# Kernel tuning notes

Measured on AMD Instinct MI355X. Metric: run time of the kernel, lower is better.

The kernel has to match this reference:

```python
import jax, jax.numpy as jnp
import numpy as np

N = 100000   # nodes
E = 1280000  # edges (avg degree ~12.8)
D = 64       # feature / hidden channels


def _init_linear(key, fan_in, fan_out):
    # Kaiming-uniform-ish init like torch Linear
    bound = 1.0 / np.sqrt(fan_in)
    return jax.random.uniform(key, (fan_in, fan_out), minval=-bound, maxval=bound)


def setup_inputs() -> dict:
    key = jax.random.key(0)
    ks = jax.random.split(key, 16)
    inp = {
        "x": jax.random.normal(ks[0], (N, D), dtype=jnp.float32),
        "edge_index": jax.random.randint(ks[1], (2, E), 0, N, dtype=jnp.int32),
        "edge_weight": jax.random.uniform(ks[2], (E,), dtype=jnp.float32),
        "batch": jnp.zeros((N,), dtype=jnp.int32),
    }
    # GraphConv params per layer: lin_rel (weight+bias) applied to aggregated
    # neighbor sum, lin_root (weight, no bias) applied to the node itself.
    for i, k in zip((1, 2, 3), range(3, 12, 3)):
        inp[f"W_rel{i}"] = _init_linear(ks[k], D, D)
        inp[f"b_rel{i}"] = jnp.zeros((D,), dtype=jnp.float32)
        inp[f"W_root{i}"] = _init_linear(ks[k + 1], D, D)
    return inp


def _graph_conv(x, src, dst, w, W_rel, b_rel, W_root):
    # message: w_ij * x_j, aggregated (sum) at target nodes
    msg = w[:, None] * x[src]                                  # [E, D]
    agg = jax.ops.segment_sum(msg, dst, num_segments=N)       # [N, D]
    return agg @ W_rel + b_rel + x @ W_root                   # [N, D]


def reference(x, edge_index, edge_weight, batch,
              W_rel1, b_rel1, W_root1,
              W_rel2, b_rel2, W_root2,
              W_rel3, b_rel3, W_root3):
    src, dst = edge_index[0], edge_index[1]
    h = jax.nn.relu(_graph_conv(x, src, dst, edge_weight, W_rel1, b_rel1, W_root1))
    h = jax.nn.relu(_graph_conv(h, src, dst, edge_weight, W_rel2, b_rel2, W_root2))
    h = _graph_conv(h, src, dst, edge_weight, W_rel3, b_rel3, W_root3)
    return h
```

## Files before the change

kernel.cpp:

```cpp
#include <hip/hip_runtime.h>
#include <hip/hip_bf16.h>

#define NN 100000
#define NE 1280000
#define DD 64
#define RSHIFT 9
#define NRANGE 196

typedef __attribute__((ext_vector_type(8))) short bf16x8;
typedef __attribute__((ext_vector_type(4))) float f32x4;

static __device__ __forceinline__ unsigned short f2bf(float f) {
    __hip_bfloat16 h = __float2bfloat16(f);
    return *reinterpret_cast<unsigned short*>(&h);
}

__global__ __launch_bounds__(256) void f32_to_bf16_kernel(
    const float* __restrict__ in, unsigned short* __restrict__ out)
{
    int i = (blockIdx.x * 256 + threadIdx.x) * 4;
    float4 v = *(const float4*)(in + i);
    ushort4 o;
    o.x = f2bf(v.x); o.y = f2bf(v.y); o.z = f2bf(v.z); o.w = f2bf(v.w);
    *(ushort4*)(out + i) = o;
}

__global__ __launch_bounds__(256) void bpack_kernel(
    const float* __restrict__ Wrel1, const float* __restrict__ Wroot1,
    const float* __restrict__ Wrel2, const float* __restrict__ Wroot2,
    const float* __restrict__ Wrel3, const float* __restrict__ Wroot3,
    unsigned short* __restrict__ Bp)
{
    int L = blockIdx.x;
    const float* Wrel  = (L == 0) ? Wrel1  : (L == 1) ? Wrel2  : Wrel3;
    const float* Wroot = (L == 0) ? Wroot1 : (L == 1) ? Wroot2 : Wroot3;
    int tid = threadIdx.x;
    int wv = tid >> 6, lane = tid & 63, quad = lane >> 4, m16 = lane & 15;
    int n = wv * 16 + m16;
    unsigned short* o = Bp + (size_t)L * 4 * 256 * 8;
#pragma unroll
    for (int t = 0; t < 4; ++t)
#pragma unroll
        for (int j = 0; j < 8; ++j) {
            int k = t * 32 + quad * 8 + j;
            float wval = (k < 64) ? Wrel[k * 64 + n] : Wroot[(k - 64) * 64 + n];
            o[((size_t)t * 256 + tid) * 8 + j] = f2bf(wval);
        }
}

__global__ __launch_bounds__(256) void hist2_kernel(
    const int* __restrict__ dst, int* __restrict__ rangeCnt)
{
    __shared__ int h[256];
    int tid = threadIdx.x;
    h[tid] = 0;
    __syncthreads();
    int e0 = blockIdx.x * 1024 + tid * 4;
    int4 d4 = *(const int4*)(dst + e0);
    atomicAdd(&h[d4.x >> RSHIFT], 1);
    atomicAdd(&h[d4.y >> RSHIFT], 1);
    atomicAdd(&h[d4.z >> RSHIFT], 1);
    atomicAdd(&h[d4.w >> RSHIFT], 1);
    __syncthreads();
    if (tid < NRANGE && h[tid]) atomicAdd(&rangeCnt[tid], h[tid]);
}

__global__ __launch_bounds__(256) void scan196_kernel(
    const int* __restrict__ rangeCnt, int* __restrict__ rangeBase,
    int* __restrict__ gcur, int* __restrict__ rowptr)
{
    __shared__ int sd[256];
    int tid = threadIdx.x;
    int v = (tid < NRANGE) ? rangeCnt[tid] : 0;
    sd[tid] = v;
    __syncthreads();
    for (int o = 1; o < 256; o <<= 1) {
        int t = (tid >= o) ? sd[tid - o] : 0;
        __syncthreads();
        sd[tid] += t;
        __syncthreads();
    }
    if (tid < NRANGE) { int ex = sd[tid] - v; rangeBase[tid] = ex; gcur[tid] = ex; }
    if (tid == 0) { rangeBase[NRANGE] = NE; rowptr[NN] = NE; }
}

__global__ __launch_bounds__(256) void p1_bin_kernel(
    const int* __restrict__ src, const int* __restrict__ dst,
    const float* __restrict__ w, int* __restrict__ gcur,
    int2* __restrict__ ecoarse)
{
    __shared__ int2 stage[1024];
    __shared__ unsigned char sbkt[1024];
    __shared__ int cnt[256], ofs[256], gpos[256], sd[256];

    int tid = threadIdx.x;
    int e0 = blockIdx.x * 1024 + tid * 4;
    int4   s4 = *(const int4*)(src + e0);
    int4   d4 = *(const int4*)(dst + e0);
    float4 w4 = *(const float4*)(w + e0);

    cnt[tid] = 0;
    __syncthreads();

    int ss[4] = {s4.x, s4.y, s4.z, s4.w};
    int dd[4] = {d4.x, d4.y, d4.z, d4.w};
    float ww[4] = {w4.x, w4.y, w4.z, w4.w};
    int b[4], p[4];
#pragma unroll
    for (int i = 0; i < 4; ++i) {
        b[i] = dd[i] >> RSHIFT;
        p[i] = atomicAdd(&cnt[b[i]], 1);
    }
    __syncthreads();

    int cv = cnt[tid];
    sd[tid] = cv;
    __syncthreads();
    for (int o = 1; o < 256; o <<= 1) {
        int t = (tid >= o) ? sd[tid - o] : 0;
        __syncthreads();
        sd[tid] += t;
        __syncthreads();
    }
    ofs[tid] = sd[tid] - cv;
    if (tid < NRANGE && cv > 0) gpos[tid] = atomicAdd(&gcur[tid], cv);
    __syncthreads();

#pragma unroll
    for (int i = 0; i < 4; ++i) {
        int slot = ofs[b[i]] + p[i];
        stage[slot] = make_int2(ss[i] | ((dd[i] & 511) << 17), __float_as_int(ww[i]));
        sbkt[slot] = (unsigned char)b[i];
    }
    __syncthreads();

    for (int j = tid; j < 1024; j += 256) {
        int bb = sbkt[j];
        ecoarse[gpos[bb] + (j - ofs[bb])] = stage[j];
    }
}

__global__ __launch_bounds__(256) void p2_place_kernel(
    const int2* __restrict__ ecoarse, const int* __restrict__ rangeBase,
    int* __restrict__ rowptr, int2* __restrict__ ebuf)
{
    __shared__ int cnt[512];
    __shared__ int ssum[256];
    int r = blockIdx.x, tid = threadIdx.x;
    int beg = rangeBase[r], end = rangeBase[r + 1];

    cnt[tid] = 0; cnt[tid + 256] = 0;
    __syncthreads();

    for (int j = beg + tid; j < end; j += 256) {
        int2 rec = ecoarse[j];
        atomicAdd(&cnt[(rec.x >> 17) & 511], 1);
    }
    __syncthreads();

    int c0 = cnt[2 * tid], c1 = cnt[2 * tid + 1];
    int s = c0 + c1;
    ssum[tid] = s;
    __syncthreads();
    for (int o = 1; o < 256; o <<= 1) {
        int t = (tid >= o) ? ssum[tid - o] : 0;
        __syncthreads();
        ssum[tid] += t;
        __syncthreads();
    }
    int p0 = beg + ssum[tid] - s;
    int p1 = p0 + c0;

    int node0 = (r << RSHIFT) + 2 * tid;
    if (node0 < NN)     rowptr[node0]     = p0;
    if (node0 + 1 < NN) rowptr[node0 + 1] = p1;
    cnt[2 * tid] = p0; cnt[2 * tid + 1] = p1;
    __syncthreads();

    for (int j = beg + tid; j < end; j += 256) {
        int2 rec = ecoarse[j];
        int dl = (rec.x >> 17) & 511;
        int p = atomicAdd(&cnt[dl], 1);
        ebuf[p] = make_int2(rec.x & 0x1FFFF, rec.y);
    }
}

template <bool RELU, bool OUT32>
__global__ __launch_bounds__(512) void fused_layer_kernel(
    const unsigned short* __restrict__ hb,
    const int* __restrict__ rowptr,
    const int2* __restrict__ ebuf,
    const unsigned short* __restrict__ Bp,
    const float* __restrict__ brel,
    void* __restrict__ outp)
{
    __shared__ __align__(16) unsigned int AstW[4 * 256];

    int tid = threadIdx.x;
    int lane = tid & 63;
    int wv = tid >> 6;
    int half = lane >> 5;
    int ch = lane & 31;
    int base = blockIdx.x * 16;
    int node = base + wv * 2 + half;

    const unsigned int* __restrict__ hw = (const unsigned int*)hb;

    bf16x8 bfrag[4];
    float bias = 0.f;
    if (wv < 4) {
#pragma unroll
        for (int t2 = 0; t2 < 4; ++t2)
            bfrag[t2] = *(const bf16x8*)(Bp + ((size_t)t2 * 256 + tid) * 8);
        bias = brel[(wv << 4) | (lane & 15)];
    }

    unsigned rootp = hw[(size_t)node * 32 + ch];

    int beg = rowptr[node];
    int end = rowptr[node + 1];
    int deg = end - beg;

    float aL0 = 0.f, aH0 = 0.f, aL1 = 0.f, aH1 = 0.f;
    for (int c = 0; c < deg; c += 32) {
        int rem = deg - c;
        int nsl = rem < 32 ? rem : 32;
        int idx = (ch < nsl) ? (c + ch) : c;
        int2 e = ebuf[beg + idx];
        float wt = (ch < nsl) ? __int_as_float(e.y) : 0.f;

        for (int s0 = 0; s0 < nsl; s0 += 8) {
#pragma unroll
            for (int i = 0; i < 8; ++i) {
                int slot = s0 + i;
                bool ok = slot < nsl;
                int sl = (half << 5) | (ok ? slot : 0);
                int sr = __shfl(e.x, sl);
                float w = __shfl(wt, sl);
                w = ok ? w : 0.f;
                unsigned v = hw[(size_t)sr * 32 + ch];
                if (i & 1) {
                    aL1 = fmaf(w, __uint_as_float(v << 16), aL1);
                    aH1 = fmaf(w, __uint_as_float(v & 0xFFFF0000u), aH1);
                } else {
                    aL0 = fmaf(w, __uint_as_float(v << 16), aL0);
                    aH0 = fmaf(w, __uint_as_float(v & 0xFFFF0000u), aH0);
                }
            }
        }
    }
    float accL = aL0 + aL1, accH = aH0 + aH1;

    int m = wv * 2 + half;
    int t = ch >> 4, q = (ch >> 2) & 3, jj = ch & 3;
    unsigned pack = ((unsigned)f2bf(accH) << 16) | (unsigned)f2bf(accL);
    AstW[t * 256 + (q * 16 + m) * 4 + jj] = pack;
    AstW[(2 + t) * 256 + (q * 16 + m) * 4 + jj] = rootp;
    __syncthreads();

    if (wv < 4) {
        int quad = lane >> 4, m16 = lane & 15;
        int n = wv * 16 + m16;
        f32x4 cacc = {0.f, 0.f, 0.f, 0.f};
#pragma unroll
        for (int t2 = 0; t2 < 4; ++t2) {
            bf16x8 a = *(const bf16x8*)&AstW[t2 * 256 + lane * 4];
            cacc = __builtin_amdgcn_mfma_f32_16x16x32_bf16(a, bfrag[t2], cacc, 0, 0, 0);
        }
#pragma unroll
        for (int reg = 0; reg < 4; ++reg) {
            int row = quad * 4 + reg;
            size_t onode = (size_t)base + row;
            float v2 = cacc[reg] + bias;
            if (RELU) v2 = fmaxf(v2, 0.f);
            if (OUT32) ((float*)outp)[onode * DD + n] = v2;
            else       ((unsigned short*)outp)[onode * DD + n] = f2bf(v2);
        }
    }
}

extern "C" void kernel_launch(void* const* d_in, const int* in_sizes, int n_in,
                              void* d_out, int out_size, void* d_ws, size_t ws_size,
                              hipStream_t stream)
{
    const float* x     = (const float*)d_in[0];
    const int*   ei    = (const int*)d_in[1];
    const float* w     = (const float*)d_in[2];
    const float* Wrel1 = (const float*)d_in[4];
    const float* brel1 = (const float*)d_in[5];
    const float* Wroot1= (const float*)d_in[6];
    const float* Wrel2 = (const float*)d_in[7];
    const float* brel2 = (const float*)d_in[8];
    const float* Wroot2= (const float*)d_in[9];
    const float* Wrel3 = (const float*)d_in[10];
    const float* brel3 = (const float*)d_in[11];
    const float* Wroot3= (const float*)d_in[12];

    float* out = (float*)d_out;

    char* ws = (char*)d_ws;
    int2*  ebuf    = (int2*)ws;                       ws += (size_t)NE * 8;
    int2*  ecoarse = (int2*)ws;
    unsigned short* xb = (unsigned short*)ws;         ws += (size_t)NN * DD * 2;
    unsigned short* hb1 = (unsigned short*)ws;        ws += (size_t)NN * DD * 2;
    unsigned short* hb2 = (unsigned short*)ws;        ws += (size_t)NN * DD * 2;
    int*   rowptr  = (int*)ws;                        ws += (size_t)(NN + 1) * 4;
    int*   rangeCnt = (int*)ws;                       ws += (size_t)256 * 4;
    int*   rangeBase = (int*)ws;                      ws += (size_t)256 * 4;
    int*   gcur    = (int*)ws;                        ws += (size_t)256 * 4;
    unsigned short* Bp = (unsigned short*)ws;

    const int* src = ei;
    const int* dst = ei + NE;

    hipMemsetAsync(rangeCnt, 0, NRANGE * 4, stream);
    bpack_kernel<<<3, 256, 0, stream>>>(Wrel1, Wroot1, Wrel2, Wroot2, Wrel3, Wroot3, Bp);
    hist2_kernel<<<1250, 256, 0, stream>>>(dst, rangeCnt);
    scan196_kernel<<<1, 256, 0, stream>>>(rangeCnt, rangeBase, gcur, rowptr);
    p1_bin_kernel<<<1250, 256, 0, stream>>>(src, dst, w, gcur, ecoarse);
    p2_place_kernel<<<NRANGE, 256, 0, stream>>>(ecoarse, rangeBase, rowptr, ebuf);

    f32_to_bf16_kernel<<<6250, 256, 0, stream>>>(x, xb);

    fused_layer_kernel<true, false><<<NN / 16, 512, 0, stream>>>(
        xb, rowptr, ebuf, Bp, brel1, hb1);
    fused_layer_kernel<true, false><<<NN / 16, 512, 0, stream>>>(
        hb1, rowptr, ebuf, Bp + (size_t)4 * 256 * 8, brel2, hb2);
    fused_layer_kernel<false, true><<<NN / 16, 512, 0, stream>>>(
        hb2, rowptr, ebuf, Bp + (size_t)8 * 256 * 8, brel3, out);
}
```

Measured before the change: 308.4 us.

## Build CSR via global degree atomics, block scan and atomic scatter

Replaces the two-pass coarse-bucket sort with a plain CSR build. The old sort staged edges in LDS and wrote them to an intermediate buffer. The new path counts per-node in-degree with global atomics, then computes row pointers with a two-level block scan. Edges are then scattered straight into their CSR slots using atomic cursors. This removes the intermediate ecoarse pass and its LDS staging, but relies on many contended global atomics and uncoalesced random writes. It also makes edge order within a row nondeterministic.

New measurement: 359.5 us. 16.5% more time.

```diff
diff --git a/kernel.cpp b/kernel.cpp
--- a/kernel.cpp
+++ b/kernel.cpp
@@ -4,8 +4,8 @@
 #define NN 100000
 #define NE 1280000
 #define DD 64
-#define RSHIFT 9
-#define NRANGE 196
+#define NBLK 98
+#define NPAD (NBLK * 1024)
 
 typedef __attribute__((ext_vector_type(8))) short bf16x8;
 typedef __attribute__((ext_vector_type(4))) float f32x4;
@@ -48,141 +48,89 @@
         }
 }
 
-__global__ __launch_bounds__(256) void hist2_kernel(
-    const int* __restrict__ dst, int* __restrict__ rangeCnt)
-{
-    __shared__ int h[256];
-    int tid = threadIdx.x;
-    h[tid] = 0;
-    __syncthreads();
-    int e0 = blockIdx.x * 1024 + tid * 4;
+__global__ __launch_bounds__(256) void degcnt_kernel(
+    const int* __restrict__ dst, int* __restrict__ deg)
+{
+    int e0 = (blockIdx.x * 256 + threadIdx.x) * 4;
     int4 d4 = *(const int4*)(dst + e0);
-    atomicAdd(&h[d4.x >> RSHIFT], 1);
-    atomicAdd(&h[d4.y >> RSHIFT], 1);
-    atomicAdd(&h[d4.z >> RSHIFT], 1);
-    atomicAdd(&h[d4.w >> RSHIFT], 1);
-    __syncthreads();
-    if (tid < NRANGE && h[tid]) atomicAdd(&rangeCnt[tid], h[tid]);
-}
-
-__global__ __launch_bounds__(256) void scan196_kernel(
-    const int* __restrict__ rangeCnt, int* __restrict__ rangeBase,
-    int* __restrict__ gcur, int* __restrict__ rowptr)
+    atomicAdd(&deg[d4.x], 1);
+    atomicAdd(&deg[d4.y], 1);
+    atomicAdd(&deg[d4.z], 1);
+    atomicAdd(&deg[d4.w], 1);
+}
+
+__global__ __launch_bounds__(256) void bsum_kernel(
+    const int* __restrict__ deg, int* __restrict__ bsum)
 {
     __shared__ int sd[256];
     int tid = threadIdx.x;
-    int v = (tid < NRANGE) ? rangeCnt[tid] : 0;
+    int4 c = *(const int4*)(deg + blockIdx.x * 1024 + tid * 4);
+    sd[tid] = c.x + c.y + c.z + c.w;
+    __syncthreads();
+    for (int o = 128; o > 0; o >>= 1) {
+        if (tid < o) sd[tid] += sd[tid + o];
+        __syncthreads();
+    }
+    if (tid == 0) bsum[blockIdx.x] = sd[0];
+}
+
+__global__ __launch_bounds__(128) void scan98_kernel(
+    const int* __restrict__ bsum, int* __restrict__ bbase,
+    int* __restrict__ rowptr)
+{
+    __shared__ int sd[128];
+    int tid = threadIdx.x;
+    int v = (tid < NBLK) ? bsum[tid] : 0;
     sd[tid] = v;
     __syncthreads();
+    for (int o = 1; o < 128; o <<= 1) {
+        int t = (tid >= o) ? sd[tid - o] : 0;
+        __syncthreads();
+        sd[tid] += t;
+        __syncthreads();
+    }
+    if (tid < NBLK) bbase[tid] = sd[tid] - v;
+    if (tid == 0) rowptr[NN] = NE;
+}
+
+__global__ __launch_bounds__(256) void bscan_kernel(
+    const int* __restrict__ deg, const int* __restrict__ bbase,
+    int* __restrict__ rowptr, int* __restrict__ cur)
+{
+    __shared__ int ssum[256];
+    int tid = threadIdx.x;
+    int n0 = blockIdx.x * 1024 + tid * 4;
+    int4 c = *(const int4*)(deg + n0);
+    int s = c.x + c.y + c.z + c.w;
+    ssum[tid] = s;
+    __syncthreads();
     for (int o = 1; o < 256; o <<= 1) {
-        int t = (tid >= o) ? sd[tid - o] : 0;
-        __syncthreads();
-        sd[tid] += t;
-        __syncthreads();
-    }
-    if (tid < NRANGE) { int ex = sd[tid] - v; rangeBase[tid] = ex; gcur[tid] = ex; }
-    if (tid == 0) { rangeBase[NRANGE] = NE; rowptr[NN] = NE; }
-}
-
-__global__ __launch_bounds__(256) void p1_bin_kernel(
+        int t = (tid >= o) ? ssum[tid - o] : 0;
+        __syncthreads();
+        ssum[tid] += t;
+        __syncthreads();
+    }
+    int base = bbase[blockIdx.x] + ssum[tid] - s;
+    int4 r;
+    r.x = base; r.y = base + c.x; r.z = r.y + c.y; r.w = r.z + c.z;
+    *(int4*)(rowptr + n0) = r;
+    *(int4*)(cur + n0) = r;
+}
+
+__global__ __launch_bounds__(256) void scatter_kernel(
     const int* __restrict__ src, const int* __restrict__ dst,
-    const float* __restrict__ w, int* __restrict__ gcur,
-    int2* __restrict__ ecoarse)
-{
-    __shared__ int2 stage[1024];
-    __shared__ unsigned char sbkt[1024];
-    __shared__ int cnt[256], ofs[256], gpos[256], sd[256];
-
-    int tid = threadIdx.x;
-    int e0 = blockIdx.x * 1024 + tid * 4;
+    const float* __restrict__ w, int* __restrict__ cur,
+    int2* __restrict__ ebuf)
+{
+    int e0 = (blockIdx.x * 256 + threadIdx.x) * 4;
     int4   s4 = *(const int4*)(src + e0);
     int4   d4 = *(const int4*)(dst + e0);
     float4 w4 = *(const float4*)(w + e0);
-
-    cnt[tid] = 0;
-    __syncthreads();
-
-    int ss[4] = {s4.x, s4.y, s4.z, s4.w};
-    int dd[4] = {d4.x, d4.y, d4.z, d4.w};
-    float ww[4] = {w4.x, w4.y, w4.z, w4.w};
-    int b[4], p[4];
-#pragma unroll
-    for (int i = 0; i < 4; ++i) {
-        b[i] = dd[i] >> RSHIFT;
-        p[i] = atomicAdd(&cnt[b[i]], 1);
-    }
-    __syncthreads();
-
-    int cv = cnt[tid];
-    sd[tid] = cv;
-    __syncthreads();
-    for (int o = 1; o < 256; o <<= 1) {
-        int t = (tid >= o) ? sd[tid - o] : 0;
-        __syncthreads();
-        sd[tid] += t;
-        __syncthreads();
-    }
-    ofs[tid] = sd[tid] - cv;
-    if (tid < NRANGE && cv > 0) gpos[tid] = atomicAdd(&gcur[tid], cv);
-    __syncthreads();
-
-#pragma unroll
-    for (int i = 0; i < 4; ++i) {
-        int slot = ofs[b[i]] + p[i];
-        stage[slot] = make_int2(ss[i] | ((dd[i] & 511) << 17), __float_as_int(ww[i]));
-        sbkt[slot] = (unsigned char)b[i];
-    }
-    __syncthreads();
-
-    for (int j = tid; j < 1024; j += 256) {
-        int bb = sbkt[j];
-        ecoarse[gpos[bb] + (j - ofs[bb])] = stage[j];
-    }
-}
-
-__global__ __launch_bounds__(256) void p2_place_kernel(
-    const int2* __restrict__ ecoarse, const int* __restrict__ rangeBase,
-    int* __restrict__ rowptr, int2* __restrict__ ebuf)
-{
-    __shared__ int cnt[512];
-    __shared__ int ssum[256];
-    int r = blockIdx.x, tid = threadIdx.x;
-    int beg = rangeBase[r], end = rangeBase[r + 1];
-
-    cnt[tid] = 0; cnt[tid + 256] = 0;
-    __syncthreads();
-
-    for (int j = beg + tid; j < end; j += 256) {
-        int2 rec = ecoarse[j];
-        atomicAdd(&cnt[(rec.x >> 17) & 511], 1);
-    }
-    __syncthreads();
-
-    int c0 = cnt[2 * tid], c1 = cnt[2 * tid + 1];
-    int s = c0 + c1;
-    ssum[tid] = s;
-    __syncthreads();
-    for (int o = 1; o < 256; o <<= 1) {
-        int t = (tid >= o) ? ssum[tid - o] : 0;
-        __syncthreads();
-        ssum[tid] += t;
-        __syncthreads();
-    }
-    int p0 = beg + ssum[tid] - s;
-    int p1 = p0 + c0;
-
-    int node0 = (r << RSHIFT) + 2 * tid;
-    if (node0 < NN)     rowptr[node0]     = p0;
-    if (node0 + 1 < NN) rowptr[node0 + 1] = p1;
-    cnt[2 * tid] = p0; cnt[2 * tid + 1] = p1;
-    __syncthreads();
-
-    for (int j = beg + tid; j < end; j += 256) {
-        int2 rec = ecoarse[j];
-        int dl = (rec.x >> 17) & 511;
-        int p = atomicAdd(&cnt[dl], 1);
-        ebuf[p] = make_int2(rec.x & 0x1FFFF, rec.y);
-    }
+    int p;
+    p = atomicAdd(&cur[d4.x], 1); ebuf[p] = make_int2(s4.x, __float_as_int(w4.x));
+    p = atomicAdd(&cur[d4.y], 1); ebuf[p] = make_int2(s4.y, __float_as_int(w4.y));
+    p = atomicAdd(&cur[d4.z], 1); ebuf[p] = make_int2(s4.z, __float_as_int(w4.z));
+    p = atomicAdd(&cur[d4.w], 1); ebuf[p] = make_int2(s4.w, __float_as_int(w4.w));
 }
 
 template <bool RELU, bool OUT32>
@@ -299,26 +247,27 @@
     float* out = (float*)d_out;
 
     char* ws = (char*)d_ws;
-    int2*  ebuf    = (int2*)ws;                       ws += (size_t)NE * 8;
-    int2*  ecoarse = (int2*)ws;
-    unsigned short* xb = (unsigned short*)ws;         ws += (size_t)NN * DD * 2;
-    unsigned short* hb1 = (unsigned short*)ws;        ws += (size_t)NN * DD * 2;
-    unsigned short* hb2 = (unsigned short*)ws;        ws += (size_t)NN * DD * 2;
-    int*   rowptr  = (int*)ws;                        ws += (size_t)(NN + 1) * 4;
-    int*   rangeCnt = (int*)ws;                       ws += (size_t)256 * 4;
-    int*   rangeBase = (int*)ws;                      ws += (size_t)256 * 4;
-    int*   gcur    = (int*)ws;                        ws += (size_t)256 * 4;
+    int2*  ebuf   = (int2*)ws;                 ws += (size_t)NE * 8;
+    unsigned short* xb  = (unsigned short*)ws; ws += (size_t)NN * DD * 2;
+    unsigned short* hb1 = (unsigned short*)ws; ws += (size_t)NN * DD * 2;
+    unsigned short* hb2 = (unsigned short*)ws; ws += (size_t)NN * DD * 2;
+    int*   rowptr = (int*)ws;                  ws += (size_t)(NPAD + 16) * 4;
+    int*   cur    = (int*)ws;                  ws += (size_t)NPAD * 4;
+    int*   deg    = (int*)ws;                  ws += (size_t)NPAD * 4;
+    int*   bsum   = (int*)ws;                  ws += (size_t)128 * 4;
+    int*   bbase  = (int*)ws;                  ws += (size_t)128 * 4;
     unsigned short* Bp = (unsigned short*)ws;
 
     const int* src = ei;
     const int* dst = ei + NE;
 
-    hipMemsetAsync(rangeCnt, 0, NRANGE * 4, stream);
+    hipMemsetAsync(deg, 0, (size_t)NPAD * 4, stream);
     bpack_kernel<<<3, 256, 0, stream>>>(Wrel1, Wroot1, Wrel2, Wroot2, Wrel3, Wroot3, Bp);
-    hist2_kernel<<<1250, 256, 0, stream>>>(dst, rangeCnt);
-    scan196_kernel<<<1, 256, 0, stream>>>(rangeCnt, rangeBase, gcur, rowptr);
-    p1_bin_kernel<<<1250, 256, 0, stream>>>(src, dst, w, gcur, ecoarse);
-    p2_place_kernel<<<NRANGE, 256, 0, stream>>>(ecoarse, rangeBase, rowptr, ebuf);
+    degcnt_kernel<<<1250, 256, 0, stream>>>(dst, deg);
+    bsum_kernel<<<NBLK, 256, 0, stream>>>(deg, bsum);
+    scan98_kernel<<<1, 128, 0, stream>>>(bsum, bbase, rowptr);
+    bscan_kernel<<<NBLK, 256, 0, stream>>>(deg, bbase, rowptr, cur);
+    scatter_kernel<<<1250, 256, 0, stream>>>(src, dst, w, cur, ebuf);
 
     f32_to_bf16_kernel<<<6250, 256, 0, stream>>>(x, xb);
 
```
